# Performance work log

Measured on AMD Instinct MI355X. Metric: run time of the kernel, lower is better.

The kernel has to match this reference:

```python
import jax, jax.numpy as jnp
import numpy as np

HDIM = 1024
CDIM = 256
TEMPER = 10.0
IGNORE_OUT = 0.0
EPS = 1e-6


def setup_inputs() -> dict:
    key = jax.random.key(0)
    ks = jax.random.split(key, 6)
    B, T, D = 2, 128, 384
    x = jax.random.normal(ks[0], (B, T, D), jnp.float32)
    y = jax.random.normal(ks[1], (B, T, D), jnp.float32)
    # xavier-normal style init for the two linear layers
    W_enc = jax.random.normal(ks[2], (D, HDIM), jnp.float32) * np.sqrt(2.0 / (D + HDIM))
    b_enc = jnp.zeros((HDIM,), jnp.float32)
    W_dec = jax.random.normal(ks[3], (HDIM, D), jnp.float32) * np.sqrt(2.0 / (D + HDIM))
    b_dec = jnp.zeros((D,), jnp.float32)
    return {"x": x, "y": y, "W_enc": W_enc, "b_enc": b_enc, "W_dec": W_dec, "b_dec": b_dec}


def reference(x, y, W_enc, b_enc, W_dec, b_dec):
    B, T, D = x.shape
    n_iter = HDIM // CDIM
    pad = D - 1
    # shift_idx[s, j] = s + j : window of width D at offset s, s in [0, 2D-2]
    shift_idx = jnp.arange(2 * D - 1)[:, None] + jnp.arange(D)[None, :]

    seq_mask = (y == IGNORE_OUT)                       # (B,T,D) bool
    denom_seq = jnp.sum(~seq_mask).astype(x.dtype)
    qn = jnp.linalg.norm(y, axis=-1)                   # (B,T)

    mask_prev = None
    x_dis, losses = [], []
    for _ in range(n_iter):
        # --- _pad_for_shift: (B,T,2D-1,D) shifted windows of x ---
        kp = jnp.pad(x, ((0, 0), (0, 0), (pad, pad)))  # (B,T,3D-2)
        kpt = kp[..., shift_idx]                       # (B,T,2D-1,D)
        # --- _score (cos) + argmax over shifts ---
        kn = jnp.linalg.norm(kpt, axis=-1)             # (B,T,2D-1)
        sim = jnp.einsum('btsd,btd->bts', kpt, y) / (qn[..., None] * kn + EPS)
        sim = jnp.where(jnp.isnan(sim), 0.0, sim)
        theta = jnp.argmax(sim, axis=-1)               # (B,T) int
        x_opt = jnp.take_along_axis(kpt, theta[..., None, None], axis=-2)[..., 0, :]  # (B,T,D)
        # --- attention: elementwise cos-scaled score, temp softmax, detached ---
        dn = (jnp.linalg.norm(x_opt, axis=-1, keepdims=True)
              * jnp.linalg.norm(y, axis=-1, keepdims=True) + EPS)
        attn = jax.nn.softmax((x_opt * y / dn) / TEMPER, axis=-1)
        attn = jnp.where(jnp.isnan(attn), 0.0, attn)
        attn = jax.lax.stop_gradient(attn)
        x_attn = x_opt * attn
        # --- _reverse_pad_for_shift: window at offset 2D-2-theta ---
        kp2 = jnp.pad(x_attn, ((0, 0), (0, 0), (pad, pad)))
        rev_idx = (2 * D - 2 - theta)[..., None] + jnp.arange(D)  # (B,T,D)
        x_ele = jnp.take_along_axis(kp2, rev_idx, axis=-1)         # (B,T,D)
        # --- self_net: encoder -> top-k sparsify -> decoder_self ---
        h = x_ele @ W_enc + b_enc                      # (B,T,HDIM)
        if mask_prev is not None:
            h = jnp.where(mask_prev > 0, 1e-10, h)
        _, idx_top = jax.lax.top_k(h, CDIM)            # (B,T,CDIM)
        flat = idx_top.reshape(B * T, CDIM)
        mask_cur = jnp.zeros((B * T, HDIM), x.dtype).at[
            jnp.arange(B * T)[:, None], flat].set(1.0).reshape(B, T, HDIM)
        if mask_prev is None:
            mask_prev = mask_cur
        else:
            mask_prev = mask_prev + mask_cur - mask_prev * mask_cur
        h = h * mask_cur
        out = h @ W_dec + b_dec                        # (B,T,D)
        x_dis.append(out)
        # --- SeqLoss (masked MSE, mean-reduced by count of valid elems) ---
        err = jnp.where(seq_mask, 0.0, (out - x) ** 2) / denom_seq
        losses.append(jnp.sum(err))
    return jnp.stack(x_dis), jnp.stack(losses)
```

## Files before the change

kernel.cpp:

```cpp
#include <hip/hip_runtime.h>
#include <hip/hip_fp16.h>
#include <math.h>

#define DD 384
#define HD 1024
#define CD 256
#define NS 765
#define NITER 4
#define NROWS 256
#define TEMPER_F 10.0f
#define EPSF 1e-6f
#define CUTF 1e-10f

typedef unsigned long long u64;
typedef unsigned int u32;
typedef _Float16 hh2 __attribute__((ext_vector_type(2)));

__device__ __forceinline__ u32 flipf(float f) {
    u32 u = __float_as_uint(f);
    return u ^ ((u32)((int)u >> 31) | 0x80000000u);
}
__device__ __forceinline__ u32 bf16r(float f) {
    u32 u = __float_as_uint(f);
    return (u + 0x7FFFu + ((u >> 16) & 1u)) >> 16;
}
__device__ __forceinline__ u32 pack2bf(float a, float b) {
    return bf16r(a) | (bf16r(b) << 16);
}
__device__ __forceinline__ float blo(u32 p) { return __uint_as_float(p << 16); }
__device__ __forceinline__ float bhi(u32 p) { return __uint_as_float(p & 0xFFFF0000u); }
__device__ __forceinline__ u32 packh2(float a, float b) {
    __half2 p = __floats2half2_rn(a, b);
    return __builtin_bit_cast(u32, p);
}
__device__ __forceinline__ float dot2(u32 a, u32 b, float c) {
#if __has_builtin(__builtin_amdgcn_fdot2)
    return __builtin_amdgcn_fdot2(__builtin_bit_cast(hh2, a),
                                  __builtin_bit_cast(hh2, b), c, false);
#else
    __half2 ah = __builtin_bit_cast(__half2, a);
    __half2 bh = __builtin_bit_cast(__half2, b);
    return fmaf(__half2float(ah.y), __half2float(bh.y),
           fmaf(__half2float(ah.x), __half2float(bh.x), c));
#endif
}

__global__ __launch_bounds__(256) void convert_kernel(
    const float* __restrict__ We, const float* __restrict__ Wd,
    u32* __restrict__ wencp, uint2* __restrict__ wd16)
{
    const int t = blockIdx.x * 256 + threadIdx.x;
    for (int i = t; i < 192 * HD; i += 65536) {
        int j2 = i >> 10, c = i & 1023;
        wencp[i] = packh2(We[(2 * j2) * HD + c], We[(2 * j2 + 1) * HD + c]);
    }
    for (int i = t; i < (HD * DD) / 4; i += 65536) {
        float4 v = ((const float4*)Wd)[i];
        wd16[i] = make_uint2(pack2bf(v.x, v.y), pack2bf(v.z, v.w));
    }
}

__global__ __launch_bounds__(1024) void fused_kernel(
    const float* __restrict__ x, const float* __restrict__ y,
    const u32* __restrict__ wencp, const float* __restrict__ benc,
    const u32* __restrict__ wdec16, const float* __restrict__ bdec,
    float* __restrict__ out_xdis, float* __restrict__ lossp,
    int* __restrict__ ycnt)
{
    const int row  = blockIdx.x;
    const int tid  = threadIdx.x;
    const int lane = tid & 63;
    const int wid  = tid >> 6;

    __shared__ __align__(16) float xpad[1152];
    __shared__ __align__(16) float yr[DD];
    __shared__ float xa[DD];
    __shared__ __align__(16) float xe_s[DD];
    __shared__ u32   xep[192];
    __shared__ __align__(16) float part[4][HD];
    __shared__ u32   sk0[HD], sk1[HD];
    __shared__ __align__(16) uint2 dec2[HD];
    __shared__ float wred[16];
    __shared__ int   wredi[16];
    __shared__ float wredn[16];
    __shared__ float s_sc[4];
    __shared__ int   s_theta;
    __shared__ u32   s_b1, s_b2, s_b3;
    __shared__ int   wcls[128];
    __shared__ int   sbase[128];
    __shared__ int   cnt8[8];
    __shared__ float loss4[NITER];

    const float* xrow = x + row * DD;
    const float* yrow = y + row * DD;

    for (int i = tid; i < 1152; i += 1024)
        xpad[i] = (i >= DD - 1 && i < 2 * DD - 1) ? xrow[i - (DD - 1)] : 0.f;
    if (tid < DD) yr[tid] = yrow[tid];
    __syncthreads();

    if (tid < DD) {
        float p = yr[tid] * yr[tid];
        int   c = (yr[tid] != 0.f) ? 1 : 0;
        for (int o = 32; o; o >>= 1) {
            p += __shfl_xor(p, o, 64);
            c += __shfl_xor(c, o, 64);
        }
        if (lane == 0) { wred[wid] = p; wredi[wid] = c; }
    }
    __syncthreads();
    if (tid == 0) {
        float s = 0.f; int c = 0;
        for (int w = 0; w < 6; ++w) { s += wred[w]; c += wredi[w]; }
        s_sc[0] = sqrtf(s);
        ycnt[row] = c;
    }
    __syncthreads();
    const float qn = s_sc[0];

    float bv = -INFINITY; int bs = 0x7fffffff; float bn = 0.f;
    if (tid < 192) {
        const float4* xp4 = (const float4*)xpad;
        const float4* yp4 = (const float4*)yr;
        float4 A = xp4[tid];
        const float f0 = A.x * A.x, f1 = A.y * A.y, f2 = A.z * A.z;
        float d0 = 0.f, d1 = 0.f, d2 = 0.f, d3 = 0.f, n0 = 0.f;
#pragma unroll 4
        for (int jc = 0; jc < 96; ++jc) {
            float4 B = xp4[tid + jc + 1];
            float4 Y = yp4[jc];
            d0 += A.x * Y.x; d0 += A.y * Y.y; d0 += A.z * Y.z; d0 += A.w * Y.w;
            d1 += A.y * Y.x; d1 += A.z * Y.y; d1 += A.w * Y.z; d1 += B.x * Y.w;
            d2 += A.z * Y.x; d2 += A.w * Y.y; d2 += B.x * Y.z; d2 += B.y * Y.w;
            d3 += A.w * Y.x; d3 += B.x * Y.y; d3 += B.y * Y.z; d3 += B.z * Y.w;
            n0 += A.x * A.x; n0 += A.y * A.y; n0 += A.z * A.z; n0 += A.w * A.w;
            A = B;
        }
        const float n1 = n0 - f0 + A.x * A.x;
        const float n2 = n1 - f1 + A.y * A.y;
        const float n3 = n2 - f2 + A.z * A.z;
        const int s0 = 4 * tid;
        float sim0 = d0 / (qn * sqrtf(n0) + EPSF);
        float sim1 = d1 / (qn * sqrtf(n1) + EPSF);
        float sim2 = d2 / (qn * sqrtf(n2) + EPSF);
        float sim3 = d3 / (qn * sqrtf(n3) + EPSF);
        bv = sim0; bs = s0; bn = n0;
        if (s0 + 1 < NS && sim1 > bv) { bv = sim1; bs = s0 + 1; bn = n1; }
        if (s0 + 2 < NS && sim2 > bv) { bv = sim2; bs = s0 + 2; bn = n2; }
        if (s0 + 3 < NS && sim3 > bv) { bv = sim3; bs = s0 + 3; bn = n3; }
    }
    for (int o = 32; o; o >>= 1) {
        float v2 = __shfl_xor(bv, o, 64);
        int   i2 = __shfl_xor(bs, o, 64);
        float n2 = __shfl_xor(bn, o, 64);
        if (v2 > bv || (v2 == bv && i2 < bs)) { bv = v2; bs = i2; bn = n2; }
    }
    if (lane == 0) { wred[wid] = bv; wredi[wid] = bs; wredn[wid] = bn; }
    __syncthreads();
    if (tid == 0) {
        float v = wred[0]; int b = wredi[0]; float nn = wredn[0];
        for (int w = 1; w < 16; ++w)
            if (wred[w] > v || (wred[w] == v && wredi[w] < b)) {
                v = wred[w]; b = wredi[w]; nn = wredn[w];
            }
        s_theta = b;
        s_sc[1] = sqrtf(nn) * qn + EPSF;
    }
    __syncthreads();
    const int theta = s_theta;
    const float dn = s_sc[1];

    float xo = 0.f, ez = 0.f;
    if (tid < DD) {
        xo = xpad[theta + tid];
        ez = expf((xo * yr[tid] / dn) / TEMPER_F);
        float p = ez;
        for (int o = 32; o; o >>= 1) p += __shfl_xor(p, o, 64);
        if (lane == 0) wred[wid] = p;
    }
    __syncthreads();
    if (tid == 0) {
        float s = 0.f;
        for (int w = 0; w < 6; ++w) s += wred[w];
        s_sc[3] = s;
    }
    __syncthreads();
    if (tid < DD) xa[tid] = xo * (ez / s_sc[3]);
    __syncthreads();
    if (tid < DD) {
        int sj = tid - (theta - (DD - 1));
        xe_s[tid] = (sj >= 0 && sj < DD) ? xa[sj] : 0.f;
    }
    __syncthreads();
    if (tid < 192) xep[tid] = packh2(xe_s[2 * tid], xe_s[2 * tid + 1]);
    __syncthreads();

    {
        const int ks = tid >> 8;
        const int c4 = tid & 255;
        const uint4* wq = (const uint4*)wencp + (size_t)(ks * 48) * 256 + c4;
        const u32* xb = xep + ks * 48;
        float4 acc = make_float4(0.f, 0.f, 0.f, 0.f);
#pragma unroll 8
        for (int j2 = 0; j2 < 48; ++j2) {
            u32 xv = xb[j2];
            uint4 w = wq[(size_t)j2 * 256];
            acc.x = dot2(xv, w.x, acc.x);
            acc.y = dot2(xv, w.y, acc.y);
            acc.z = dot2(xv, w.z, acc.z);
            acc.w = dot2(xv, w.w, acc.w);
        }
        *(float4*)&part[ks][4 * c4] = acc;
    }
    if (tid < 8) cnt8[tid] = 0;
    if (tid < NITER) loss4[tid] = 0.f;
    __syncthreads();

    float oh;
    u32 okey, e;
    {
        oh = part[0][tid] + part[1][tid] + part[2][tid] + part[3][tid] + benc[tid];
        okey = ~flipf(oh);
        e = okey;
    }

    int par = 0;
    for (int k = 2; k <= HD; k <<= 1) {
        const bool up = (tid & k) == 0;
        for (int j = k >> 1; j > 0; j >>= 1) {
            if (j <= 32) {
                u32 p = __shfl_xor(e, j, 64);
                const bool takeMin = ((tid & j) == 0) == up;
                e = takeMin ? (e < p ? e : p) : (e > p ? e : p);
            } else {
                u32* buf = par ? sk1 : sk0; par ^= 1;
                buf[tid] = e;
                __syncthreads();
                u32 p = buf[tid ^ j];
                const bool takeMin = ((tid & j) == 0) == up;
                e = takeMin ? (e < p ? e : p) : (e > p ? e : p);
            }
        }
    }
    if (tid == 255) s_b1 = e;
    if (tid == 511) s_b2 = e;
    if (tid == 767) s_b3 = e;
    __syncthreads();
    const u32 b1 = s_b1, b2 = s_b2, b3 = s_b3;

    {
        const int myk = (okey <= b1) ? 0 : (okey <= b2) ? 1 : (okey <= b3) ? 2 : 3;
        const int cls = 2 * myk + ((oh > CUTF) ? 0 : 1);
        int myprefix = 0;
        const u64 ltmask = (1ull << lane) - 1;
#pragma unroll
        for (int c = 0; c < 8; ++c) {
            u64 m = __ballot(cls == c);
            if (cls == c) myprefix = __popcll(m & ltmask);
            if (lane == 0) {
                wcls[c * 16 + wid] = (int)__popcll(m);
                atomicAdd(&cnt8[c], (int)__popcll(m));
            }
        }
        __syncthreads();
        if (tid < 128) {
            int v = wcls[tid];
            int inc = v;
            for (int o = 1; o < 64; o <<= 1) {
                int t2 = __shfl_up(inc, o, 64);
                if (lane >= o) inc += t2;
            }
            sbase[tid] = inc - v;
        }
        __syncthreads();
        if (tid >= 64 && tid < 128) sbase[tid] += sbase[63] + wcls[63];
        __syncthreads();
        const int slot = sbase[cls * 16 + wid] + myprefix;
        dec2[slot] = make_uint2(__float_as_uint(oh), (u32)tid * 192u);
    }
    __syncthreads();

    {
        const int k = tid >> 8;
        const int g = tid & 255;
        const bool active = (g < 192);
        int n = 0;
        if (active) n = (k == 0) ? CD : cnt8[2 * k];
        float2 oacc = make_float2(0.f, 0.f);
        if (active) oacc = *(const float2*)&bdec[2 * g];
        const u32* wd = wdec16 + g;
        const int base = k * CD;
        int r = 0;
        for (; r + 8 <= n; r += 8) {
#pragma unroll
            for (int q = 0; q < 8; q += 2) {
                uint4 dv = *(const uint4*)&dec2[base + r + q];
                float v0 = __uint_as_float(dv.x);
                u32 w0 = wd[dv.y];
                float v1 = __uint_as_float(dv.z);
                u32 w1 = wd[dv.w];
                oacc.x += v0 * blo(w0); oacc.y += v0 * bhi(w0);
                oacc.x += v1 * blo(w1); oacc.y += v1 * bhi(w1);
            }
        }
        for (; r < n; ++r) {
            uint2 dv = dec2[base + r];
            float v0 = __uint_as_float(dv.x);
            u32 w0 = wd[dv.y];
            oacc.x += v0 * blo(w0); oacc.y += v0 * bhi(w0);
        }
        float l = 0.f;
        if (active) {
            *(float2*)&out_xdis[((size_t)k * NROWS + row) * DD + 2 * g] = oacc;
            float2 xv = *(const float2*)&xrow[2 * g];
            float2 yv = *(const float2*)&yr[2 * g];
            float ee;
            ee = oacc.x - xv.x; if (yv.x != 0.f) l += ee * ee;
            ee = oacc.y - xv.y; if (yv.y != 0.f) l += ee * ee;
        }
        for (int o = 32; o; o >>= 1) l += __shfl_xor(l, o, 64);
        if (lane == 0) atomicAdd(&loss4[k], l);
    }
    __syncthreads();
    if (tid < NITER) lossp[row * NITER + tid] = loss4[tid];
}

__global__ __launch_bounds__(256) void finalize2(
    const float* __restrict__ lossp, const int* __restrict__ ycnt,
    float* __restrict__ losses)
{
    const int tid = threadIdx.x, lane = tid & 63, w = tid >> 6;
    __shared__ int ctot[4];
    int c = ycnt[tid];
    for (int o = 32; o; o >>= 1) c += __shfl_xor(c, o, 64);
    if (lane == 0) ctot[w] = c;
    __syncthreads();
    const int total = ctot[0] + ctot[1] + ctot[2] + ctot[3];
    float s = lossp[lane * NITER + w] + lossp[(lane + 64) * NITER + w]
            + lossp[(lane + 128) * NITER + w] + lossp[(lane + 192) * NITER + w];
    for (int o = 32; o; o >>= 1) s += __shfl_xor(s, o, 64);
    if (lane == 0) losses[w] = s / (float)total;
}

extern "C" void kernel_launch(void* const* d_in, const int* in_sizes, int n_in,
                              void* d_out, int out_size, void* d_ws, size_t ws_size,
                              hipStream_t stream) {
    const float* x    = (const float*)d_in[0];
    const float* y    = (const float*)d_in[1];
    const float* Wenc = (const float*)d_in[2];
    const float* benc = (const float*)d_in[3];
    const float* Wdec = (const float*)d_in[4];
    const float* bdec = (const float*)d_in[5];

    float* out  = (float*)d_out;
    float* loss = out + (out_size - NITER);

    float* lossp  = (float*)d_ws;
    int*   ycnt   = (int*)(lossp + NROWS * NITER);
    u32*   wencp  = (u32*)(ycnt + NROWS);
    u32*   wdec16 = wencp + 192 * HD;

    convert_kernel<<<256, 256, 0, stream>>>(Wenc, Wdec, wencp, (uint2*)wdec16);
    fused_kernel<<<NROWS, 1024, 0, stream>>>(x, y, wencp, benc, wdec16, bdec,
                                             out, lossp, ycnt);
    finalize2<<<1, 256, 0, stream>>>(lossp, ycnt, loss);
}
```

Baseline: 106.2 us.

## Split decoder rows across thread halves and fuse loss finalize via ticket

The sparse decoder stage now has each thread own four output columns and process half of the selected hidden units. Partial sums go through shared memory and are added in a second pass that also writes outputs and computes the masked loss, so all 1024 threads do useful work instead of 768. The separate finalize kernel is removed: loss sums and valid counts are accumulated with global atomics, and the last block, found through an atomic ticket, writes the final losses. This saves a kernel launch but adds fences, global atomics, a shared-memory reduction pass and nondeterministic float summation order.

New measurement: 168.6 us. +58.8%, slower.

```diff
diff --git a/kernel.cpp b/kernel.cpp
--- a/kernel.cpp
+++ b/kernel.cpp
@@ -47,8 +47,9 @@
 
 __global__ __launch_bounds__(256) void convert_kernel(
     const float* __restrict__ We, const float* __restrict__ Wd,
-    u32* __restrict__ wencp, uint2* __restrict__ wd16)
+    u32* __restrict__ hdr, u32* __restrict__ wencp, uint2* __restrict__ wd16)
 {
+    if (blockIdx.x == 0 && threadIdx.x < 8) hdr[threadIdx.x] = 0;
     const int t = blockIdx.x * 256 + threadIdx.x;
     for (int i = t; i < 192 * HD; i += 65536) {
         int j2 = i >> 10, c = i & 1023;
@@ -64,8 +65,9 @@
     const float* __restrict__ x, const float* __restrict__ y,
     const u32* __restrict__ wencp, const float* __restrict__ benc,
     const u32* __restrict__ wdec16, const float* __restrict__ bdec,
-    float* __restrict__ out_xdis, float* __restrict__ lossp,
-    int* __restrict__ ycnt)
+    float* __restrict__ out_xdis, float* __restrict__ gloss,
+    int* __restrict__ gcnt, int* __restrict__ ticket,
+    float* __restrict__ losses)
 {
     const int row  = blockIdx.x;
     const int tid  = threadIdx.x;
@@ -80,6 +82,7 @@
     __shared__ __align__(16) float part[4][HD];
     __shared__ u32   sk0[HD], sk1[HD];
     __shared__ __align__(16) uint2 dec2[HD];
+    __shared__ __align__(16) float4 dpart[8][96];
     __shared__ float wred[16];
     __shared__ int   wredi[16];
     __shared__ float wredn[16];
@@ -113,7 +116,7 @@
         float s = 0.f; int c = 0;
         for (int w = 0; w < 6; ++w) { s += wred[w]; c += wredi[w]; }
         s_sc[0] = sqrtf(s);
-        ycnt[row] = c;
+        atomicAdd(gcnt, c);
     }
     __syncthreads();
     const float qn = s_sc[0];
@@ -281,65 +284,89 @@
     __syncthreads();
 
     {
-        const int k = tid >> 8;
-        const int g = tid & 255;
-        const bool active = (g < 192);
+        const int g8 = tid >> 7;
+        const int k  = g8 >> 1;
+        const int hf = g8 & 1;
+        const int gg = tid & 127;
+        const bool active = (gg < 96);
         int n = 0;
         if (active) n = (k == 0) ? CD : cnt8[2 * k];
-        float2 oacc = make_float2(0.f, 0.f);
-        if (active) oacc = *(const float2*)&bdec[2 * g];
-        const u32* wd = wdec16 + g;
+        int r  = hf * 128;
+        int r1 = n < r + 128 ? n : r + 128;
+        if (r1 < r) r1 = r;
+        float4 acc = make_float4(0.f, 0.f, 0.f, 0.f);
+        const u32* wd = wdec16 + 2 * gg;
         const int base = k * CD;
-        int r = 0;
-        for (; r + 8 <= n; r += 8) {
+        for (; r + 8 <= r1; r += 8) {
 #pragma unroll
             for (int q = 0; q < 8; q += 2) {
                 uint4 dv = *(const uint4*)&dec2[base + r + q];
                 float v0 = __uint_as_float(dv.x);
-                u32 w0 = wd[dv.y];
+                uint2 w0 = *(const uint2*)(wd + dv.y);
                 float v1 = __uint_as_float(dv.z);
-                u32 w1 = wd[dv.w];
-                oacc.x += v0 * blo(w0); oacc.y += v0 * bhi(w0);
-                oacc.x += v1 * blo(w1); oacc.y += v1 * bhi(w1);
-            }
-        }
-        for (; r < n; ++r) {
+                uint2 w1 = *(const uint2*)(wd + dv.w);
+                acc.x += v0 * blo(w0.x); acc.y += v0 * bhi(w0.x);
+                acc.z += v0 * blo(w0.y); acc.w += v0 * bhi(w0.y);
+                acc.x += v1 * blo(w1.x); acc.y += v1 * bhi(w1.x);
+                acc.z += v1 * blo(w1.y); acc.w += v1 * bhi(w1.y);
+            }
+        }
+        for (; r < r1; ++r) {
             uint2 dv = dec2[base + r];
             float v0 = __uint_as_float(dv.x);
-            u32 w0 = wd[dv.y];
-            oacc.x += v0 * blo(w0); oacc.y += v0 * bhi(w0);
-        }
+            uint2 w0 = *(const uint2*)(wd + dv.y);
+            acc.x += v0 * blo(w0.x); acc.y += v0 * bhi(w0.x);
+            acc.z += v0 * blo(w0.y); acc.w += v0 * bhi(w0.y);
+        }
+        if (active) dpart[g8][gg] = acc;
+    }
+    __syncthreads();
+
+    {
         float l = 0.f;
-        if (active) {
-            *(float2*)&out_xdis[((size_t)k * NROWS + row) * DD + 2 * g] = oacc;
-            float2 xv = *(const float2*)&xrow[2 * g];
-            float2 yv = *(const float2*)&yr[2 * g];
-            float ee;
-            ee = oacc.x - xv.x; if (yv.x != 0.f) l += ee * ee;
-            ee = oacc.y - xv.y; if (yv.y != 0.f) l += ee * ee;
+        if (tid < 512) {
+            const int k2 = tid >> 7;
+            const int q  = tid & 127;
+            if (q < 96) {
+                float4 a = dpart[2 * k2][q];
+                float4 b = dpart[2 * k2 + 1][q];
+                float4 bb = *(const float4*)&bdec[4 * q];
+                float4 o4;
+                o4.x = a.x + b.x + bb.x;
+                o4.y = a.y + b.y + bb.y;
+                o4.z = a.z + b.z + bb.z;
+                o4.w = a.w + b.w + bb.w;
+                *(float4*)&out_xdis[((size_t)k2 * NROWS + row) * DD + 4 * q] = o4;
+                float4 xv = *(const float4*)&xrow[4 * q];
+                float4 yv = *(const float4*)&yr[4 * q];
+                float ee;
+                ee = o4.x - xv.x; if (yv.x != 0.f) l += ee * ee;
+                ee = o4.y - xv.y; if (yv.y != 0.f) l += ee * ee;
+                ee = o4.z - xv.z; if (yv.z != 0.f) l += ee * ee;
+                ee = o4.w - xv.w; if (yv.w != 0.f) l += ee * ee;
+            }
         }
         for (int o = 32; o; o >>= 1) l += __shfl_xor(l, o, 64);
-        if (lane == 0) atomicAdd(&loss4[k], l);
-    }
-    __syncthreads();
-    if (tid < NITER) lossp[row * NITER + tid] = loss4[tid];
-}
-
-__global__ __launch_bounds__(256) void finalize2(
-    const float* __restrict__ lossp, const int* __restrict__ ycnt,
-    float* __restrict__ losses)
-{
-    const int tid = threadIdx.x, lane = tid & 63, w = tid >> 6;
-    __shared__ int ctot[4];
-    int c = ycnt[tid];
-    for (int o = 32; o; o >>= 1) c += __shfl_xor(c, o, 64);
-    if (lane == 0) ctot[w] = c;
-    __syncthreads();
-    const int total = ctot[0] + ctot[1] + ctot[2] + ctot[3];
-    float s = lossp[lane * NITER + w] + lossp[(lane + 64) * NITER + w]
-            + lossp[(lane + 128) * NITER + w] + lossp[(lane + 192) * NITER + w];
-    for (int o = 32; o; o >>= 1) s += __shfl_xor(s, o, 64);
-    if (lane == 0) losses[w] = s / (float)total;
+        if (tid < 512 && lane == 0) atomicAdd(&loss4[tid >> 7], l);
+    }
+    __syncthreads();
+
+    if (tid < NITER) atomicAdd(&gloss[tid], loss4[tid]);
+    __threadfence();
+    __syncthreads();
+    if (tid == 0) {
+        int t = __hip_atomic_fetch_add(ticket, 1, __ATOMIC_ACQ_REL,
+                                       __HIP_MEMORY_SCOPE_AGENT);
+        if (t == NROWS - 1) {
+            int total = __hip_atomic_load(gcnt, __ATOMIC_RELAXED,
+                                          __HIP_MEMORY_SCOPE_AGENT);
+            for (int k = 0; k < NITER; ++k) {
+                float s = __hip_atomic_load(&gloss[k], __ATOMIC_RELAXED,
+                                            __HIP_MEMORY_SCOPE_AGENT);
+                losses[k] = s / (float)total;
+            }
+        }
+    }
 }
 
 extern "C" void kernel_launch(void* const* d_in, const int* in_sizes, int n_in,
@@ -355,13 +382,14 @@
     float* out  = (float*)d_out;
     float* loss = out + (out_size - NITER);
 
-    float* lossp  = (float*)d_ws;
-    int*   ycnt   = (int*)(lossp + NROWS * NITER);
-    u32*   wencp  = (u32*)(ycnt + NROWS);
+    float* gloss  = (float*)d_ws;
+    int*   gcnt   = (int*)d_ws + 4;
+    int*   ticket = (int*)d_ws + 5;
+    u32*   wencp  = (u32*)d_ws + 16;
     u32*   wdec16 = wencp + 192 * HD;
 
-    convert_kernel<<<256, 256, 0, stream>>>(Wenc, Wdec, wencp, (uint2*)wdec16);
+    convert_kernel<<<256, 256, 0, stream>>>(Wenc, Wdec, (u32*)d_ws, wencp,
+                                            (uint2*)wdec16);
     fused_kernel<<<NROWS, 1024, 0, stream>>>(x, y, wencp, benc, wdec16, bdec,
-                                             out, lossp, ycnt);
-    finalize2<<<1, 256, 0, stream>>>(lossp, ycnt, loss);
-}
+                                             out, gloss, gcnt, ticket, loss);
+}
```
